# Performance work log

Measured on AMD Instinct MI355X. Metric: run time of the kernel, lower is better.

Reference implementation:

```python
import jax, jax.numpy as jnp
import numpy as np
from jax import lax

FEAT_STRIDE = 16
NMS_THRESH = 0.7
N_PRE = 6000   # test-mode n_test_pre_nms
N_POST = 300   # test-mode n_test_post_nms
MIN_SIZE = 16.0
SCALE = 1.0
RATIOS = (0.5, 1.0, 2.0)
ANCHOR_SCALES = (8, 16, 32)
BASE = 16
N_ANCHOR = len(RATIOS) * len(ANCHOR_SCALES)  # 9


def _anchor_base():
    py = px = BASE / 2.0
    ab = np.zeros((N_ANCHOR, 4), np.float32)
    for i, r in enumerate(RATIOS):
        for j, s in enumerate(ANCHOR_SCALES):
            h = BASE * s * np.sqrt(r)
            w = BASE * s * np.sqrt(1.0 / r)
            k = i * len(ANCHOR_SCALES) + j
            ab[k] = [py - h / 2.0, px - w / 2.0, py + h / 2.0, px + w / 2.0]
    return ab


def _anchors(hh, ww):
    # enumerate_shifted_anchor: (y1,x1,y2,x2) anchors for every feature cell
    ab = _anchor_base()
    sy = np.arange(0, hh * FEAT_STRIDE, FEAT_STRIDE)
    sx = np.arange(0, ww * FEAT_STRIDE, FEAT_STRIDE)
    SX, SY = np.meshgrid(sx, sy)
    shift = np.stack([SY.ravel(), SX.ravel(), SY.ravel(), SX.ravel()], 1)
    anc = (ab[None, :, :] + shift[:, None, :]).reshape(-1, 4).astype(np.float32)
    return jnp.asarray(anc)


def _iou(b):
    # b: [N,4] (y1,x1,y2,x2) -> [N,N] IoU
    y1, x1, y2, x2 = b[:, 0], b[:, 1], b[:, 2], b[:, 3]
    area = (y2 - y1) * (x2 - x1)
    ih = jnp.clip(jnp.minimum(y2[:, None], y2[None, :]) - jnp.maximum(y1[:, None], y1[None, :]), 0.0)
    iw = jnp.clip(jnp.minimum(x2[:, None], x2[None, :]) - jnp.maximum(x1[:, None], x1[None, :]), 0.0)
    inter = ih * iw
    return inter / (area[:, None] + area[None, :] - inter + 1e-9)


def _propose(loc, fg, anchor, img_h, img_w):
    # loc:[M,4] fg:[M] anchor:[M,4]  -> padded [N_POST,4] rois + valid mask
    ah = anchor[:, 2] - anchor[:, 0]
    aw = anchor[:, 3] - anchor[:, 1]
    acy = anchor[:, 0] + 0.5 * ah
    acx = anchor[:, 1] + 0.5 * aw
    cy = loc[:, 0] * ah + acy
    cx = loc[:, 1] * aw + acx
    h = jnp.exp(loc[:, 2]) * ah
    w = jnp.exp(loc[:, 3]) * aw
    roi = jnp.stack([
        jnp.clip(cy - 0.5 * h, 0.0, img_h),
        jnp.clip(cx - 0.5 * w, 0.0, img_w),
        jnp.clip(cy + 0.5 * h, 0.0, img_h),
        jnp.clip(cx + 0.5 * w, 0.0, img_w),
    ], axis=1)
    hs = roi[:, 2] - roi[:, 0]
    ws = roi[:, 3] - roi[:, 1]
    ms = MIN_SIZE * SCALE
    valid = (hs >= ms) & (ws >= ms)
    sc = jnp.where(valid, fg, -jnp.inf)  # drop too-small boxes from ranking
    top_sc, idx = lax.top_k(sc, N_PRE)   # score-sorted pre-NMS candidates
    boxes = roi[idx]
    ok = lax.stop_gradient(jnp.isfinite(top_sc))
    sup = lax.stop_gradient(_iou(boxes) > NMS_THRESH)  # [N_PRE,N_PRE]
    tri = jnp.arange(N_PRE)

    def body(i, keep):
        suppressed = jnp.any(keep & sup[:, i] & (tri < i))
        return keep.at[i].set(ok[i] & ~suppressed)

    keep = lax.fori_loop(0, N_PRE, body, jnp.zeros((N_PRE,), bool))
    rank = jnp.cumsum(keep.astype(jnp.int32)) - 1
    sel = keep & (rank < N_POST)
    tgt = jnp.where(sel, rank, N_POST)  # N_POST is out-of-bounds -> dropped
    out = jnp.zeros((N_POST, 4), boxes.dtype).at[tgt].set(boxes, mode='drop')
    vmask = jnp.zeros((N_POST,), bool).at[tgt].set(True, mode='drop')
    return out, vmask


def reference(x, conv1_w, conv1_b, score_w, score_b, loc_w, loc_b, img_h, img_w):
    n, _, hh, ww = x.shape
    anchor = _anchors(hh, ww)
    h = jax.nn.relu(
        lax.conv_general_dilated(x, conv1_w, (1, 1), 'SAME',
                                 dimension_numbers=('NCHW', 'OIHW', 'NCHW'))
        + conv1_b[None, :, None, None])
    locs = jnp.einsum('nchw,oc->nohw', h, loc_w[:, :, 0, 0]) + loc_b[None, :, None, None]
    scr = jnp.einsum('nchw,oc->nohw', h, score_w[:, :, 0, 0]) + score_b[None, :, None, None]
    rpn_locs = locs.transpose(0, 2, 3, 1).reshape(n, -1, 4)          # [n,M,4]
    scr_t = scr.transpose(0, 2, 3, 1)                                 # [n,hh,ww,2A]
    soft = jax.nn.softmax(scr_t.reshape(n, hh, ww, N_ANCHOR, 2), axis=-1)
    fg = soft[..., 1].reshape(n, -1)                                  # [n,M]
    rpn_scores = scr_t.reshape(n, -1, 2)
    rois, vmask = jax.vmap(lambda l, f: _propose(l, f, anchor, img_h, img_w))(rpn_locs, fg)
    roi_indices = jnp.broadcast_to(jnp.arange(n, dtype=jnp.int32)[:, None], (n, N_POST))
    return rpn_locs, rpn_scores, rois, roi_indices, anchor, vmask


def setup_inputs() -> dict:
    key = jax.random.key(0)
    ks = jax.random.split(key, 4)
    x = jax.random.normal(ks[0], (2, 512, 64, 64), jnp.float32)
    conv1_w = 0.01 * jax.random.normal(ks[1], (512, 512, 3, 3), jnp.float32)
    conv1_b = jnp.zeros((512,), jnp.float32)
    score_w = 0.01 * jax.random.normal(ks[2], (N_ANCHOR * 2, 512, 1, 1), jnp.float32)
    score_b = jnp.zeros((N_ANCHOR * 2,), jnp.float32)
    loc_w = 0.01 * jax.random.normal(ks[3], (N_ANCHOR * 4, 512, 1, 1), jnp.float32)
    loc_b = jnp.zeros((N_ANCHOR * 4,), jnp.float32)
    return {"x": x, "conv1_w": conv1_w, "conv1_b": conv1_b,
            "score_w": score_w, "score_b": score_b,
            "loc_w": loc_w, "loc_b": loc_b,
            "img_h": 1024, "img_w": 1024}
```

## Files before the change

kernel.cpp:

```cpp
#include <hip/hip_runtime.h>
#include <hip/hip_bf16.h>
#include <math.h>
#include <cstdint>

typedef unsigned long long u64;
typedef unsigned int u32;
typedef _Float16 half8 __attribute__((ext_vector_type(8)));
typedef float floatx4 __attribute__((ext_vector_type(4)));

#define NANCH 36864
#define SEG 65536
#define N_PRE 6000
#define N_POST 300
#define NW 96
#define NPADC 6144

#define O0 0
#define O1 294912
#define O2 442368
#define O3 444768
#define O4 445368
#define O5 592824

#define WS_XHI   0
#define WS_XLO   2097152
#define WS_WHI   4194304
#define WS_WLO   5373952
#define WS_WSLT  6553600
#define WS_WSLB  6586368
#define WS_H     6586432
#define WS_GUARD 10780736
#define WS_FG    0
#define WS_ROI   73728
#define WS_KEYS  368640
#define WS_SBOX  630784
#define WS_ALIVE 679936
#define WS_MASK  4194304

#define HSCALE 9.5367431640625e-07f

__device__ __forceinline__ void gl_lds16(const void* g, void* l) {
  __builtin_amdgcn_global_load_lds(
      (const __attribute__((address_space(1))) u32*)g,
      (__attribute__((address_space(3))) u32*)l, 16, 0, 0);
}

__device__ __forceinline__ u64 bcast64(u64 v, int src) {
  u32 lo = (u32)__shfl((int)(v & 0xFFFFFFFFull), src);
  u32 hi = (u32)__shfl((int)(v >> 32), src);
  return ((u64)hi << 32) | lo;
}

__global__ __launch_bounds__(256) void prep_all(
    const float* __restrict__ x, const float* __restrict__ w,
    const float* __restrict__ lw, const float* __restrict__ sw,
    const float* __restrict__ lb, const float* __restrict__ sb,
    float4* __restrict__ h, float4* __restrict__ guard,
    _Float16* __restrict__ xhi, _Float16* __restrict__ xlo,
    _Float16* __restrict__ whi, _Float16* __restrict__ wlo,
    float* __restrict__ wslt, float* __restrict__ wslb) {
  __shared__ float s[64 * 65];
  const int b = blockIdx.x, tid = threadIdx.x;
  if (b < 4097) {
    int idx = b * 256 + tid;
    if (idx < 1048576) h[idx] = make_float4(0.f, 0.f, 0.f, 0.f);
    else if (idx < 1048576 + 16) guard[idx - 1048576] = make_float4(0.f, 0.f, 0.f, 0.f);
    return;
  }
  if (b < 5121) {
    int l = b - 4097;
    int pt = l & 63, cg = (l >> 6) & 7, n = l >> 9;
    const int c0 = cg << 6, p0 = pt << 6;
#pragma unroll
    for (int kk = 0; kk < 16; ++kk) {
      int e = tid + (kk << 8);
      int ci = e >> 6, pi = e & 63;
      s[ci * 65 + pi] = x[(((size_t)(n * 512 + c0 + ci)) << 12) + p0 + pi];
    }
    __syncthreads();
#pragma unroll
    for (int kk = 0; kk < 16; ++kk) {
      int e = tid + (kk << 8);
      int ci = e & 63, pi = e >> 6;
      float sv = s[ci * 65 + pi] * 1024.f;
      _Float16 hi = (_Float16)sv;
      _Float16 lo = (_Float16)(sv - (float)hi);
      size_t off = (((size_t)(n << 12) + p0 + pi) << 9) + c0 + ci;
      xhi[off] = hi;
      xlo[off] = lo;
    }
    return;
  }
  if (b < 5697) {
    int l = b - 5121;
    int ct = l & 7, ot = (l >> 3) & 7, t = l >> 6;
    const int c0 = ct << 6, o0 = ot << 6;
#pragma unroll
    for (int kk = 0; kk < 16; ++kk) {
      int e = tid + (kk << 8);
      int ci = e & 63, oi = e >> 6;
      float sv = w[(size_t)(o0 + oi) * 4608 + (c0 + ci) * 9 + t] * 1024.f;
      _Float16 hi = (_Float16)sv;
      _Float16 lo = (_Float16)(sv - (float)hi);
      size_t off = ((size_t)((t << 9) + o0 + oi) << 9) + c0 + ci;
      whi[off] = hi;
      wlo[off] = lo;
    }
    return;
  }
  {
    int e = (b - 5697) * 256 + tid;
    if (e < 32768) {
      int c = e >> 6, o = e & 63;
      float v = 0.f;
      if (o < 36) v = lw[o * 512 + c];
      else if (o < 54) v = sw[(o - 36) * 512 + c];
      wslt[e] = v;
    } else if (e < 32832) {
      int o = e - 32768;
      float v = 0.f;
      if (o < 36) v = lb[o];
      else if (o < 54) v = sb[o - 36];
      wslb[o] = v;
    }
  }
}

__global__ __launch_bounds__(256) void conv_mfma(
    const _Float16* __restrict__ xhi, const _Float16* __restrict__ xlo,
    const _Float16* __restrict__ whi, const _Float16* __restrict__ wlo,
    const float* __restrict__ guard, float* __restrict__ hout) {
  __shared__ _Float16 aHi[4 * 68 * 32];
  __shared__ _Float16 aLo[4 * 68 * 32];
  __shared__ _Float16 bHi[128 * 32];
  __shared__ _Float16 bLo[128 * 32];
  const int tid = threadIdx.x;
  const int lane = tid & 63, w = tid >> 6;
  const int ptile = blockIdx.x;
  const int og = blockIdx.y;
  const int kq = blockIdx.z;
  const int n = ptile >> 5;
  const int y0 = (ptile & 31) << 1;
  const int o0 = og << 7;
  const int l15 = lane & 15, l16 = lane >> 4;
  const int ry = w >> 1;
  const int wo = (w & 1) << 6;

  floatx4 acc[4][4];
#pragma unroll
  for (int a = 0; a < 4; ++a)
#pragma unroll
    for (int b = 0; b < 4; ++b) acc[a][b] = (floatx4)0.f;

  for (int s = 0; s < 8; ++s) {
    const int c0 = (kq << 8) + (s << 5);
    __syncthreads();
    for (int i = w; i < 17; i += 4) {
      int chunk = (i << 6) + lane;
      int p = chunk >> 2, q = chunk & 3;
      int r = p / 68, xs = p - r * 68;
      int y = y0 - 1 + r, xg = xs - 1;
      bool ok = ((unsigned)y < 64u) && ((unsigned)xg < 64u);
      size_t off = (((size_t)(n << 12) + (y << 6) + xg) << 9) + c0 + (q << 3);
      const void* gh = ok ? (const void*)(xhi + off) : (const void*)guard;
      const void* gl = ok ? (const void*)(xlo + off) : (const void*)guard;
      gl_lds16(gh, (char*)aHi + (i << 10));
      gl_lds16(gl, (char*)aLo + (i << 10));
    }
    for (int tt = 0; tt < 9; ++tt) {
      if (tt > 0) __syncthreads();
      for (int i = w; i < 8; i += 4) {
        int chunk = (i << 6) + lane;
        int row = chunk >> 2, q = chunk & 3;
        size_t off = ((size_t)((tt << 9) + o0 + row) << 9) + c0 + (q << 3);
        gl_lds16((const void*)(whi + off), (char*)bHi + (i << 10));
        gl_lds16((const void*)(wlo + off), (char*)bLo + (i << 10));
      }
      __syncthreads();

      const int dy = tt / 3, dx = tt - 3 * dy;
      half8 ah[4], al[4], bh[4], bl[4];
#pragma unroll
      for (int im = 0; im < 4; ++im) {
        int xp = (im << 4) + l15;
        int p = (ry + dy) * 68 + xp + dx;
        ah[im] = *(const half8*)&aHi[(p << 5) + (l16 << 3)];
        al[im] = *(const half8*)&aLo[(p << 5) + (l16 << 3)];
      }
#pragma unroll
      for (int in = 0; in < 4; ++in) {
        int orow = wo + (in << 4) + l15;
        bh[in] = *(const half8*)&bHi[(orow << 5) + (l16 << 3)];
        bl[in] = *(const half8*)&bLo[(orow << 5) + (l16 << 3)];
      }
#pragma unroll
      for (int im = 0; im < 4; ++im)
#pragma unroll
        for (int in = 0; in < 4; ++in) {
          acc[im][in] = __builtin_amdgcn_mfma_f32_16x16x32_f16(
              ah[im], bh[in], acc[im][in], 0, 0, 0);
          acc[im][in] = __builtin_amdgcn_mfma_f32_16x16x32_f16(
              ah[im], bl[in], acc[im][in], 0, 0, 0);
          acc[im][in] = __builtin_amdgcn_mfma_f32_16x16x32_f16(
              al[im], bh[in], acc[im][in], 0, 0, 0);
        }
    }
  }

#pragma unroll
  for (int im = 0; im < 4; ++im)
#pragma unroll
    for (int in = 0; in < 4; ++in) {
      int o = o0 + wo + (in << 4) + l15;
#pragma unroll
      for (int reg = 0; reg < 4; ++reg) {
        int m_local = (ry << 6) + (im << 4) + (l16 << 2) + reg;
        size_t off = (((size_t)(n << 12) + (y0 << 6) + m_local) << 9) + o;
        atomicAdd(&hout[off], acc[im][in][reg]);
      }
    }
}

__global__ __launch_bounds__(256) void head_kernel(
    const float* __restrict__ hbuf, const float* __restrict__ cb,
    const float* __restrict__ wslt, const float* __restrict__ wslb,
    float* __restrict__ out, float* __restrict__ fgbuf) {
  const int y = blockIdx.x, n = blockIdx.y;
  __shared__ float sH[16 * 65];
  __shared__ float sWt[1024];
  __shared__ float sOut[64 * 65];
  const int tid = threadIdx.x;
  const int x = tid & 63, og = tid >> 6;

  float acc[16];
#pragma unroll
  for (int j = 0; j < 16; ++j) acc[j] = 0.f;

  const float* hb = hbuf + (((size_t)(n << 12) + (y << 6)) << 9);

  for (int c0 = 0; c0 < 512; c0 += 16) {
    __syncthreads();
#pragma unroll
    for (int p = 0; p < 4; ++p) {
      int e = tid + (p << 8);
      {
        int cc = e & 15, xx = e >> 4;
        float raw = hb[((size_t)xx << 9) + c0 + cc];
        sH[cc * 65 + xx] = fmaxf(raw * HSCALE + cb[c0 + cc], 0.f);
      }
      {
        int cc = e >> 6, xx = e & 63;
        sWt[e] = wslt[((c0 + cc) << 6) + xx];
      }
    }
    __syncthreads();
#pragma unroll
    for (int cc = 0; cc < 16; ++cc) {
      float hv = sH[cc * 65 + x];
      const float4* wp = (const float4*)&sWt[(cc << 6) + (og << 4)];
      float4 w0 = wp[0], w1 = wp[1], w2 = wp[2], w3 = wp[3];
      acc[0]  = fmaf(hv, w0.x, acc[0]);  acc[1]  = fmaf(hv, w0.y, acc[1]);
      acc[2]  = fmaf(hv, w0.z, acc[2]);  acc[3]  = fmaf(hv, w0.w, acc[3]);
      acc[4]  = fmaf(hv, w1.x, acc[4]);  acc[5]  = fmaf(hv, w1.y, acc[5]);
      acc[6]  = fmaf(hv, w1.z, acc[6]);  acc[7]  = fmaf(hv, w1.w, acc[7]);
      acc[8]  = fmaf(hv, w2.x, acc[8]);  acc[9]  = fmaf(hv, w2.y, acc[9]);
      acc[10] = fmaf(hv, w2.z, acc[10]); acc[11] = fmaf(hv, w2.w, acc[11]);
      acc[12] = fmaf(hv, w3.x, acc[12]); acc[13] = fmaf(hv, w3.y, acc[13]);
      acc[14] = fmaf(hv, w3.z, acc[14]); acc[15] = fmaf(hv, w3.w, acc[15]);
    }
  }
  __syncthreads();
#pragma unroll
  for (int j = 0; j < 16; ++j) {
    int o = (og << 4) + j;
    sOut[o * 65 + x] = acc[j] + wslb[o];
  }
  __syncthreads();

  const int p0 = (n << 12) + (y << 6);
  float* locs = out + O0 + (size_t)p0 * 36;
  for (int e = tid; e < 2304; e += 256) {
    int xx = e / 36, o = e - xx * 36;
    locs[e] = sOut[o * 65 + xx];
  }
  float* scrs = out + O1 + (size_t)p0 * 18;
  for (int e = tid; e < 1152; e += 256) {
    int xx = e / 18, ss = e - xx * 18;
    scrs[e] = sOut[(36 + ss) * 65 + xx];
  }
  float* fg = fgbuf + n * NANCH + (y << 6) * 9;
  for (int e = tid; e < 576; e += 256) {
    int xx = e / 9, a = e - xx * 9;
    float s0 = sOut[(36 + 2 * a) * 65 + xx];
    float s1 = sOut[(36 + 2 * a + 1) * 65 + xx];
    fg[e] = 1.0f / (1.0f + expf(s0 - s1));
  }
}

__global__ __launch_bounds__(256) void decode_kernel(
    const float* __restrict__ out0, const float* __restrict__ fgbuf,
    float4* __restrict__ roibuf, u64* __restrict__ keys,
    float* __restrict__ anchor_out, float* __restrict__ out,
    const int* __restrict__ imgh_p, const int* __restrict__ imgw_p) {
  int gid = blockIdx.x * 256 + threadIdx.x;
  if (gid < 3600) {
    if (gid < 2400) out[O2 + gid] = 0.f;
    else if (gid < 3000) out[O3 + (gid - 2400)] = (float)((gid - 2400) / 300);
    else out[O5 + (gid - 3000)] = 0.f;
  }
  int n = gid >> 16, k = gid & (SEG - 1);
  if (k >= NANCH) { keys[gid] = ~0ull; return; }
  int a = k % 9;
  int p = k / 9;
  int py = p >> 6, px = p & 63;

  const double R[3] = {0.5, 1.0, 2.0};
  const double S[3] = {8.0, 16.0, 32.0};
  double r = R[a / 3], s = S[a - (a / 3) * 3];
  double hd = 16.0 * s * sqrt(r);
  double wd = 16.0 * s * sqrt(1.0 / r);
  float ay1 = (float)(8.0 - hd / 2.0) + (float)(py * 16);
  float ax1 = (float)(8.0 - wd / 2.0) + (float)(px * 16);
  float ay2 = (float)(8.0 + hd / 2.0) + (float)(py * 16);
  float ax2 = (float)(8.0 + wd / 2.0) + (float)(px * 16);
  if (n == 0) {
    float* ao = anchor_out + (size_t)k * 4;
    ao[0] = ay1; ao[1] = ax1; ao[2] = ay2; ao[3] = ax2;
  }
  float ahk = ay2 - ay1, awk = ax2 - ax1;
  float acy = ay1 + 0.5f * ahk, acx = ax1 + 0.5f * awk;
  const float* lp = out0 + ((size_t)(n * NANCH + k) << 2);
  float dy = lp[0], dx = lp[1], dh = lp[2], dw = lp[3];
  float cy = dy * ahk + acy;
  float cx = dx * awk + acx;
  float bh = expf(dh) * ahk;
  float bw = expf(dw) * awk;
  float img_h = (float)imgh_p[0], img_w = (float)imgw_p[0];
  float y1 = fminf(fmaxf(cy - 0.5f * bh, 0.f), img_h);
  float x1 = fminf(fmaxf(cx - 0.5f * bw, 0.f), img_w);
  float y2 = fminf(fmaxf(cy + 0.5f * bh, 0.f), img_h);
  float x2 = fminf(fmaxf(cx + 0.5f * bw, 0.f), img_w);
  bool valid = ((y2 - y1) >= 16.f) && ((x2 - x1) >= 16.f);
  float sc = valid ? fgbuf[n * NANCH + k] : -INFINITY;
  roibuf[n * NANCH + k] = make_float4(y1, x1, y2, x2);
  unsigned int b = __float_as_uint(sc);
  unsigned int m = b ^ ((b & 0x80000000u) ? 0xFFFFFFFFu : 0x80000000u);
  keys[gid] = ((u64)(~m) << 32) | (unsigned int)k;
}

__global__ __launch_bounds__(256) void sort_local_a(u64* __restrict__ keys) {
  __shared__ u64 sk[4096];
  const int base = blockIdx.x << 12;
  for (int e = threadIdx.x; e < 4096; e += 256) sk[e] = keys[base + e];
  __syncthreads();
  for (int k = 2; k <= 4096; k <<= 1) {
    for (int j = k >> 1; j > 0; j >>= 1) {
      for (int t = threadIdx.x; t < 2048; t += 256) {
        int l = ((t & ~(j - 1)) << 1) | (t & (j - 1));
        int rr = l | j;
        bool asc = (((base + l) & k) == 0);
        u64 a = sk[l], b = sk[rr];
        if ((a > b) == asc) { sk[l] = b; sk[rr] = a; }
      }
      __syncthreads();
    }
  }
  for (int e = threadIdx.x; e < 4096; e += 256) keys[base + e] = sk[e];
}

__global__ __launch_bounds__(256) void sort_global_pass(u64* __restrict__ keys,
                                                        int k, int j) {
  int t = blockIdx.x * 256 + threadIdx.x;
  int l = ((t & ~(j - 1)) << 1) | (t & (j - 1));
  int rr = l | j;
  bool asc = (((l & (SEG - 1)) & k) == 0);
  u64 a = keys[l], b = keys[rr];
  if ((a > b) == asc) { keys[l] = b; keys[rr] = a; }
}

__global__ __launch_bounds__(256) void sort_global_pass2(u64* __restrict__ keys,
                                                         int k, int j1) {
  int t = blockIdx.x * 256 + threadIdx.x;
  int j2 = j1 >> 1;
  int l = ((t & ~(j2 - 1)) << 1) | (t & (j2 - 1));
  l = ((l & ~(j1 - 1)) << 1) | (l & (j1 - 1));
  u64 e0 = keys[l], e1 = keys[l | j2], e2 = keys[l | j1], e3 = keys[l | j1 | j2];
  bool asc = (((l & (SEG - 1)) & k) == 0);
  u64 tmp;
  if ((e0 > e2) == asc) { tmp = e0; e0 = e2; e2 = tmp; }
  if ((e1 > e3) == asc) { tmp = e1; e1 = e3; e3 = tmp; }
  if ((e0 > e1) == asc) { tmp = e0; e0 = e1; e1 = tmp; }
  if ((e2 > e3) == asc) { tmp = e2; e2 = e3; e3 = tmp; }
  keys[l] = e0; keys[l | j2] = e1; keys[l | j1] = e2; keys[l | j1 | j2] = e3;
}

__global__ __launch_bounds__(256) void sort_local_b(u64* __restrict__ keys, int k) {
  __shared__ u64 sk[4096];
  const int base = blockIdx.x << 12;
  for (int e = threadIdx.x; e < 4096; e += 256) sk[e] = keys[base + e];
  __syncthreads();
  for (int j = 2048; j > 0; j >>= 1) {
    for (int t = threadIdx.x; t < 2048; t += 256) {
      int l = ((t & ~(j - 1)) << 1) | (t & (j - 1));
      int rr = l | j;
      bool asc = ((((base + l) & (SEG - 1)) & k) == 0);
      u64 a = sk[l], b = sk[rr];
      if ((a > b) == asc) { sk[l] = b; sk[rr] = a; }
    }
    __syncthreads();
  }
  for (int e = threadIdx.x; e < 4096; e += 256) keys[base + e] = sk[e];
}

__global__ __launch_bounds__(256) void nms_gather(
    const u64* __restrict__ keys, const float4* __restrict__ roibuf,
    float4* __restrict__ sbox, u64* __restrict__ alive) {
  const int n = blockIdx.y;
  int i = blockIdx.x * 256 + threadIdx.x;
  u64 kk = (i < N_PRE) ? keys[(n << 16) + i] : ~0ull;
  bool valid = ((unsigned)(kk >> 32)) < 0xFF800000u;
  float4 b = make_float4(0.f, 0.f, 0.f, 0.f);
  if (valid) b = roibuf[(size_t)n * NANCH + (unsigned)(kk & 0xFFFFFFFFull)];
  sbox[n * NPADC + i] = b;
  u64 bal = __ballot(valid);
  if ((threadIdx.x & 63) == 0) alive[n * NW + (i >> 6)] = bal;
}

__global__ __launch_bounds__(256) void build_mask(
    const float4* __restrict__ sbox, u64* __restrict__ M) {
  __shared__ float4 jb[4][64];
  __shared__ float ja[4][64];
  const int tid = threadIdx.x, lane = tid & 63, wv = tid >> 6;
  const int g = blockIdx.x, q = blockIdx.y, n = blockIdx.z;
  const float4* sb = sbox + n * NPADC;
  float4 bi = sb[(g << 6) + lane];
  float ai = (bi.z - bi.x) * (bi.w - bi.y);
  u64* Mrow = M + ((size_t)(n * NPADC + (g << 6) + lane)) * NW;
#pragma unroll
  for (int it = 0; it < 6; ++it) {
    int w = q * 24 + (it << 2) + wv;
    float4 bjl = sb[(w << 6) + lane];
    jb[wv][lane] = bjl;
    ja[wv][lane] = (bjl.z - bjl.x) * (bjl.w - bjl.y);
    u64 bits = 0;
#pragma unroll 8
    for (int j = 0; j < 64; ++j) {
      float4 bj = jb[wv][j];
      float aj = ja[wv][j];
      float ih = fmaxf(fminf(bi.z, bj.z) - fmaxf(bi.x, bj.x), 0.f);
      float iw = fmaxf(fminf(bi.w, bj.w) - fmaxf(bi.y, bj.y), 0.f);
      float inter = ih * iw;
      bool bit = inter / (ai + aj - inter + 1e-9f) > 0.7f;
      bits |= ((u64)bit) << j;
    }
    Mrow[w] = bits;
  }
}

__global__ __launch_bounds__(64) void nms_reduce(
    const u64* __restrict__ M, const u64* __restrict__ alive,
    const float4* __restrict__ sbox, float* __restrict__ out) {
  const int n = blockIdx.x, lane = threadIdx.x;
  float* rois = out + O2 + n * (N_POST * 4);
  float* vmask = out + O5 + n * N_POST;
  const u64* A = alive + n * NW;
  const u64* Mb = M + (size_t)n * NPADC * NW;
  const float4* sb = sbox + n * NPADC;
  u64 aw0 = A[lane];
  u64 aw1 = (lane < 32) ? A[64 + lane] : 0ull;
  u64 accA = 0, accB = 0;
  int nk = 0;
  u64 dnext = Mb[(size_t)lane * NW + 0];
  float4 bnext = sb[lane];
  const u64 below = lane ? (~0ull >> (64 - lane)) : 0ull;

  for (int c = 0; c < 94; ++c) {
    u64 dcur = dnext;
    float4 bcur = bnext;
    if (c + 1 < 94) {
      dnext = Mb[(size_t)(((c + 1) << 6) + lane) * NW + (c + 1)];
      bnext = sb[((c + 1) << 6) + lane];
    }
    u64 wacc = (c < 64) ? bcast64(accA, c) : bcast64(accB, c - 64);
    u64 aw = (c < 64) ? bcast64(aw0, c) : bcast64(aw1, c - 64);
    u64 alive_u = aw & ~wacc;
    if (alive_u == 0ull) continue;

    u64 dmask = dcur & below;
    u64 rem = alive_u, kept = 0;
    while (rem) {
      int j = __builtin_ctzll(rem);
      kept |= 1ull << j;
      u64 col = __ballot((dmask >> j) & 1);
      rem &= ~(col | (1ull << j));
    }

    int npop = __popcll(kept);
    if ((kept >> lane) & 1ull) {
      int slot = nk + __popcll(kept & below);
      if (slot < N_POST) {
        rois[slot * 4 + 0] = bcur.x; rois[slot * 4 + 1] = bcur.y;
        rois[slot * 4 + 2] = bcur.z; rois[slot * 4 + 3] = bcur.w;
        vmask[slot] = 1.0f;
      }
    }
    if (nk + npop >= N_POST) break;
    nk += npop;

    u64 kk = kept;
    while (kk) {
      int j0 = __builtin_ctzll(kk); kk &= kk - 1;
      int j1 = kk ? __builtin_ctzll(kk) : j0; kk &= kk - 1;
      int j2 = kk ? __builtin_ctzll(kk) : j0; kk &= kk - 1;
      int j3 = kk ? __builtin_ctzll(kk) : j0; kk &= kk - 1;
      int j4 = kk ? __builtin_ctzll(kk) : j0; kk &= kk - 1;
      int j5 = kk ? __builtin_ctzll(kk) : j0; kk &= kk - 1;
      int j6 = kk ? __builtin_ctzll(kk) : j0; kk &= kk - 1;
      int j7 = kk ? __builtin_ctzll(kk) : j0; kk &= kk - 1;
      const u64* r0 = Mb + (size_t)((c << 6) + j0) * NW;
      const u64* r1 = Mb + (size_t)((c << 6) + j1) * NW;
      const u64* r2 = Mb + (size_t)((c << 6) + j2) * NW;
      const u64* r3 = Mb + (size_t)((c << 6) + j3) * NW;
      const u64* r4 = Mb + (size_t)((c << 6) + j4) * NW;
      const u64* r5 = Mb + (size_t)((c << 6) + j5) * NW;
      const u64* r6 = Mb + (size_t)((c << 6) + j6) * NW;
      const u64* r7 = Mb + (size_t)((c << 6) + j7) * NW;
      u64 oA = r0[lane] | r1[lane] | r2[lane] | r3[lane]
             | r4[lane] | r5[lane] | r6[lane] | r7[lane];
      u64 oB = 0;
      if (lane < 32)
        oB = r0[64 + lane] | r1[64 + lane] | r2[64 + lane] | r3[64 + lane]
           | r4[64 + lane] | r5[64 + lane] | r6[64 + lane] | r7[64 + lane];
      accA |= oA;
      accB |= oB;
    }
  }
}

extern "C" void kernel_launch(void* const* d_in, const int* in_sizes, int n_in,
                              void* d_out, int out_size, void* d_ws, size_t ws_size,
                              hipStream_t stream) {
  const float* x        = (const float*)d_in[0];
  const float* conv1_w  = (const float*)d_in[1];
  const float* conv1_b  = (const float*)d_in[2];
  const float* score_w  = (const float*)d_in[3];
  const float* score_b  = (const float*)d_in[4];
  const float* loc_w    = (const float*)d_in[5];
  const float* loc_b    = (const float*)d_in[6];
  const int*   imgh_p   = (const int*)d_in[7];
  const int*   imgw_p   = (const int*)d_in[8];

  float* out = (float*)d_out;
  float* ws  = (float*)d_ws;

  _Float16* xhi = (_Float16*)(ws + WS_XHI);
  _Float16* xlo = (_Float16*)(ws + WS_XLO);
  _Float16* whi = (_Float16*)(ws + WS_WHI);
  _Float16* wlo = (_Float16*)(ws + WS_WLO);
  float* wslt   = ws + WS_WSLT;
  float* wslb   = ws + WS_WSLB;
  float* hbuf   = ws + WS_H;
  float* guard  = ws + WS_GUARD;
  float* fgbuf   = ws + WS_FG;
  float4* roibuf = (float4*)(ws + WS_ROI);
  u64* keys      = (u64*)(ws + WS_KEYS);
  float4* sbox   = (float4*)(ws + WS_SBOX);
  u64* alive     = (u64*)(ws + WS_ALIVE);
  u64* maskbuf   = (u64*)(ws + WS_MASK);

  prep_all<<<5826, 256, 0, stream>>>(x, conv1_w, loc_w, score_w, loc_b, score_b,
                                     (float4*)hbuf, (float4*)guard,
                                     xhi, xlo, whi, wlo, wslt, wslb);

  conv_mfma<<<dim3(64, 4, 2), 256, 0, stream>>>(xhi, xlo, whi, wlo, guard, hbuf);

  head_kernel<<<dim3(64, 2), 256, 0, stream>>>(hbuf, conv1_b, wslt, wslb, out, fgbuf);
  decode_kernel<<<512, 256, 0, stream>>>(out, fgbuf, roibuf, keys,
                                         out + O4, out, imgh_p, imgw_p);

  sort_local_a<<<32, 256, 0, stream>>>(keys);
  for (int k = 8192; k <= SEG; k <<= 1) {
    int j = k >> 1;
    while (j >= 4096) {
      if (j >= 8192) {
        sort_global_pass2<<<128, 256, 0, stream>>>(keys, k, j);
        j >>= 2;
      } else {
        sort_global_pass<<<256, 256, 0, stream>>>(keys, k, j);
        j >>= 1;
      }
    }
    sort_local_b<<<32, 256, 0, stream>>>(keys, k);
  }

  nms_gather<<<dim3(24, 2), 256, 0, stream>>>(keys, roibuf, sbox, alive);
  build_mask<<<dim3(96, 4, 2), 256, 0, stream>>>(sbox, maskbuf);
  nms_reduce<<<2, 64, 0, stream>>>(maskbuf, alive, sbox, out);
}
```

Measured before the change: 499.2 us.

## Replace full bitonic sort with histogram top-k select; swizzle conv LDS, split-K 4

Swaps the multi-launch 65536-element global bitonic sort for a pass that builds a radix histogram of score keys, scans it to find the cutoff bin for the top 6000, compacts the survivors and sorts 8192 keys in one LDS block per image, gathering boxes in the same kernel. Separately, the conv kernel splits the reduction over 4 K-chunks instead of 2 and XOR-style swizzles the LDS layout to cut bank conflicts. The head kernel now uses float4 loads and zeroes the histogram and key buffers. This removes many kernel launches and a lot of global-memory sort traffic. In exchange it adds more atomics on the conv output and relies on at most 8192 candidates falling at or below the cutoff bin, so ties could be truncated.

```diff
diff --git a/kernel.cpp b/kernel.cpp
--- a/kernel.cpp
+++ b/kernel.cpp
@@ -35,6 +35,10 @@
 #define WS_KEYS  368640
 #define WS_SBOX  630784
 #define WS_ALIVE 679936
+#define WS_CKEYS 680320
+#define WS_CNT   717184
+#define WS_CUT   717248
+#define WS_HIST2 2097152
 #define WS_MASK  4194304
 
 #define HSCALE 9.5367431640625e-07f
@@ -139,8 +143,8 @@
   const int ptile = blockIdx.x;
   const int og = blockIdx.y;
   const int kq = blockIdx.z;
-  const int n = ptile >> 5;
   const int y0 = (ptile & 31) << 1;
+  const int nimg = ptile >> 5;
   const int o0 = og << 7;
   const int l15 = lane & 15, l16 = lane >> 4;
   const int ry = w >> 1;
@@ -152,16 +156,17 @@
 #pragma unroll
     for (int b = 0; b < 4; ++b) acc[a][b] = (floatx4)0.f;
 
-  for (int s = 0; s < 8; ++s) {
-    const int c0 = (kq << 8) + (s << 5);
+  for (int s = 0; s < 4; ++s) {
+    const int c0 = (kq << 7) + (s << 5);
     __syncthreads();
     for (int i = w; i < 17; i += 4) {
       int chunk = (i << 6) + lane;
-      int p = chunk >> 2, q = chunk & 3;
+      int p = chunk >> 2;
+      int q = ((chunk & 3) - ((chunk >> 3) & 3)) & 3;
       int r = p / 68, xs = p - r * 68;
       int y = y0 - 1 + r, xg = xs - 1;
       bool ok = ((unsigned)y < 64u) && ((unsigned)xg < 64u);
-      size_t off = (((size_t)(n << 12) + (y << 6) + xg) << 9) + c0 + (q << 3);
+      size_t off = (((size_t)(nimg << 12) + (y << 6) + xg) << 9) + c0 + (q << 3);
       const void* gh = ok ? (const void*)(xhi + off) : (const void*)guard;
       const void* gl = ok ? (const void*)(xlo + off) : (const void*)guard;
       gl_lds16(gh, (char*)aHi + (i << 10));
@@ -171,7 +176,8 @@
       if (tt > 0) __syncthreads();
       for (int i = w; i < 8; i += 4) {
         int chunk = (i << 6) + lane;
-        int row = chunk >> 2, q = chunk & 3;
+        int row = chunk >> 2;
+        int q = ((chunk & 3) - ((chunk >> 3) & 3)) & 3;
         size_t off = ((size_t)((tt << 9) + o0 + row) << 9) + c0 + (q << 3);
         gl_lds16((const void*)(whi + off), (char*)bHi + (i << 10));
         gl_lds16((const void*)(wlo + off), (char*)bLo + (i << 10));
@@ -183,15 +189,17 @@
 #pragma unroll
       for (int im = 0; im < 4; ++im) {
         int xp = (im << 4) + l15;
-        int p = (ry + dy) * 68 + xp + dx;
-        ah[im] = *(const half8*)&aHi[(p << 5) + (l16 << 3)];
-        al[im] = *(const half8*)&aLo[(p << 5) + (l16 << 3)];
+        int P = (ry + dy) * 68 + xp + dx;
+        int sw = ((l16 + (P >> 1)) & 3) << 3;
+        ah[im] = *(const half8*)&aHi[(P << 5) + sw];
+        al[im] = *(const half8*)&aLo[(P << 5) + sw];
       }
 #pragma unroll
       for (int in = 0; in < 4; ++in) {
         int orow = wo + (in << 4) + l15;
-        bh[in] = *(const half8*)&bHi[(orow << 5) + (l16 << 3)];
-        bl[in] = *(const half8*)&bLo[(orow << 5) + (l16 << 3)];
+        int swb = ((l16 + (orow >> 1)) & 3) << 3;
+        bh[in] = *(const half8*)&bHi[(orow << 5) + swb];
+        bl[in] = *(const half8*)&bLo[(orow << 5) + swb];
       }
 #pragma unroll
       for (int im = 0; im < 4; ++im)
@@ -215,7 +223,7 @@
 #pragma unroll
       for (int reg = 0; reg < 4; ++reg) {
         int m_local = (ry << 6) + (im << 4) + (l16 << 2) + reg;
-        size_t off = (((size_t)(n << 12) + (y0 << 6) + m_local) << 9) + o;
+        size_t off = (((size_t)(nimg << 12) + (y0 << 6) + m_local) << 9) + o;
         atomicAdd(&hout[off], acc[im][in][reg]);
       }
     }
@@ -224,13 +232,25 @@
 __global__ __launch_bounds__(256) void head_kernel(
     const float* __restrict__ hbuf, const float* __restrict__ cb,
     const float* __restrict__ wslt, const float* __restrict__ wslb,
-    float* __restrict__ out, float* __restrict__ fgbuf) {
+    float* __restrict__ out, float* __restrict__ fgbuf,
+    float4* __restrict__ zkeys, float4* __restrict__ zhist,
+    float4* __restrict__ zcnt) {
   const int y = blockIdx.x, n = blockIdx.y;
   __shared__ float sH[16 * 65];
   __shared__ float sWt[1024];
   __shared__ float sOut[64 * 65];
   const int tid = threadIdx.x;
   const int x = tid & 63, og = tid >> 6;
+  const int bb = (n << 6) + y;
+
+  {
+    float f = __uint_as_float(0xFFFFFFFFu);
+    if (tid < 64) zkeys[(bb << 6) + tid] = make_float4(f, f, f, f);
+#pragma unroll
+    for (int i = 0; i < 4; ++i)
+      zhist[(bb << 10) + (i << 8) + tid] = make_float4(0.f, 0.f, 0.f, 0.f);
+    if (bb == 0 && tid < 16) zcnt[tid] = make_float4(0.f, 0.f, 0.f, 0.f);
+  }
 
   float acc[16];
 #pragma unroll
@@ -238,20 +258,17 @@
 
   const float* hb = hbuf + (((size_t)(n << 12) + (y << 6)) << 9);
 
+  const int cc4 = (tid & 3) << 2, xx = tid >> 2;
   for (int c0 = 0; c0 < 512; c0 += 16) {
     __syncthreads();
-#pragma unroll
-    for (int p = 0; p < 4; ++p) {
-      int e = tid + (p << 8);
-      {
-        int cc = e & 15, xx = e >> 4;
-        float raw = hb[((size_t)xx << 9) + c0 + cc];
-        sH[cc * 65 + xx] = fmaxf(raw * HSCALE + cb[c0 + cc], 0.f);
-      }
-      {
-        int cc = e >> 6, xx = e & 63;
-        sWt[e] = wslt[((c0 + cc) << 6) + xx];
-      }
+    {
+      float4 v = *(const float4*)&hb[((size_t)xx << 9) + c0 + cc4];
+      float4 bbv = *(const float4*)&cb[c0 + cc4];
+      sH[(cc4 + 0) * 65 + xx] = fmaxf(v.x * HSCALE + bbv.x, 0.f);
+      sH[(cc4 + 1) * 65 + xx] = fmaxf(v.y * HSCALE + bbv.y, 0.f);
+      sH[(cc4 + 2) * 65 + xx] = fmaxf(v.z * HSCALE + bbv.z, 0.f);
+      sH[(cc4 + 3) * 65 + xx] = fmaxf(v.w * HSCALE + bbv.w, 0.f);
+      *(float4*)&sWt[tid << 2] = *(const float4*)&wslt[(c0 << 6) + (tid << 2)];
     }
     __syncthreads();
 #pragma unroll
@@ -280,19 +297,19 @@
   const int p0 = (n << 12) + (y << 6);
   float* locs = out + O0 + (size_t)p0 * 36;
   for (int e = tid; e < 2304; e += 256) {
-    int xx = e / 36, o = e - xx * 36;
-    locs[e] = sOut[o * 65 + xx];
+    int xp = e / 36, o = e - xp * 36;
+    locs[e] = sOut[o * 65 + xp];
   }
   float* scrs = out + O1 + (size_t)p0 * 18;
   for (int e = tid; e < 1152; e += 256) {
-    int xx = e / 18, ss = e - xx * 18;
-    scrs[e] = sOut[(36 + ss) * 65 + xx];
+    int xp = e / 18, ss = e - xp * 18;
+    scrs[e] = sOut[(36 + ss) * 65 + xp];
   }
   float* fg = fgbuf + n * NANCH + (y << 6) * 9;
   for (int e = tid; e < 576; e += 256) {
-    int xx = e / 9, a = e - xx * 9;
-    float s0 = sOut[(36 + 2 * a) * 65 + xx];
-    float s1 = sOut[(36 + 2 * a + 1) * 65 + xx];
+    int xp = e / 9, a = e - xp * 9;
+    float s0 = sOut[(36 + 2 * a) * 65 + xp];
+    float s1 = sOut[(36 + 2 * a + 1) * 65 + xp];
     fg[e] = 1.0f / (1.0f + expf(s0 - s1));
   }
 }
@@ -301,15 +318,18 @@
     const float* __restrict__ out0, const float* __restrict__ fgbuf,
     float4* __restrict__ roibuf, u64* __restrict__ keys,
     float* __restrict__ anchor_out, float* __restrict__ out,
+    u32* __restrict__ ghist,
     const int* __restrict__ imgh_p, const int* __restrict__ imgw_p) {
-  int gid = blockIdx.x * 256 + threadIdx.x;
+  const int tid = threadIdx.x, bb = blockIdx.x;
+  const int n = bb / 144;
+  const int k = (bb - n * 144) * 256 + tid;
+  int gid = bb * 256 + tid;
   if (gid < 3600) {
     if (gid < 2400) out[O2 + gid] = 0.f;
     else if (gid < 3000) out[O3 + (gid - 2400)] = (float)((gid - 2400) / 300);
     else out[O5 + (gid - 3000)] = 0.f;
   }
-  int n = gid >> 16, k = gid & (SEG - 1);
-  if (k >= NANCH) { keys[gid] = ~0ull; return; }
+
   int a = k % 9;
   int p = k / 9;
   int py = p >> 6, px = p & 63;
@@ -345,85 +365,83 @@
   roibuf[n * NANCH + k] = make_float4(y1, x1, y2, x2);
   unsigned int b = __float_as_uint(sc);
   unsigned int m = b ^ ((b & 0x80000000u) ? 0xFFFFFFFFu : 0x80000000u);
-  keys[gid] = ((u64)(~m) << 32) | (unsigned int)k;
-}
-
-__global__ __launch_bounds__(256) void sort_local_a(u64* __restrict__ keys) {
-  __shared__ u64 sk[4096];
-  const int base = blockIdx.x << 12;
-  for (int e = threadIdx.x; e < 4096; e += 256) sk[e] = keys[base + e];
+  u32 hi = ~m;
+  keys[(n << 16) + k] = ((u64)hi << 32) | (unsigned int)k;
+  atomicAdd(&ghist[(n << 18) + (hi >> 14)], 1u);
+}
+
+__global__ __launch_bounds__(1024) void scan_cut(const u32* __restrict__ ghist,
+                                                 u32* __restrict__ cut) {
+  __shared__ u32 ps[1024];
+  const int n = blockIdx.x, tid = threadIdx.x;
+  const u32* h = ghist + (n << 18);
+  u32 s = 0;
+  const uint4* h4 = (const uint4*)(h + (tid << 8));
+#pragma unroll
+  for (int i = 0; i < 64; ++i) {
+    uint4 v = h4[i];
+    s += v.x + v.y + v.z + v.w;
+  }
+  ps[tid] = s;
   __syncthreads();
-  for (int k = 2; k <= 4096; k <<= 1) {
+  for (int off = 1; off < 1024; off <<= 1) {
+    u32 v = (tid >= off) ? ps[tid - off] : 0;
+    __syncthreads();
+    ps[tid] += v;
+    __syncthreads();
+  }
+  u32 cumEnd = ps[tid], cumStart = cumEnd - s;
+  if (cumStart < N_PRE && cumEnd >= N_PRE) {
+    u32 c = cumStart;
+    for (int i = 0; i < 256; ++i) {
+      c += h[(tid << 8) + i];
+      if (c >= N_PRE) { cut[n] = (tid << 8) + i; break; }
+    }
+  }
+}
+
+__global__ __launch_bounds__(256) void compact(
+    const u64* __restrict__ keys, const u32* __restrict__ cut,
+    u32* __restrict__ cnt, u64* __restrict__ ckeys) {
+  const int b = blockIdx.x;
+  const int n = b / 144;
+  const int k = (b - n * 144) * 256 + threadIdx.x;
+  u64 key = keys[(n << 16) + k];
+  u32 bin = (u32)(key >> 46);
+  if (bin <= cut[n]) {
+    u32 pos = atomicAdd(&cnt[n], 1u);
+    if (pos < 8192) ckeys[(n << 13) + pos] = key;
+  }
+}
+
+__global__ __launch_bounds__(1024) void sort8k(
+    const u64* __restrict__ ckeys, const float4* __restrict__ roibuf,
+    float4* __restrict__ sbox, u64* __restrict__ alive) {
+  __shared__ u64 sk[8192];
+  const int n = blockIdx.x, tid = threadIdx.x;
+  for (int i = tid; i < 8192; i += 1024) sk[i] = ckeys[(n << 13) + i];
+  __syncthreads();
+  for (int k = 2; k <= 8192; k <<= 1) {
     for (int j = k >> 1; j > 0; j >>= 1) {
-      for (int t = threadIdx.x; t < 2048; t += 256) {
+      for (int t = tid; t < 4096; t += 1024) {
         int l = ((t & ~(j - 1)) << 1) | (t & (j - 1));
         int rr = l | j;
-        bool asc = (((base + l) & k) == 0);
+        bool asc = ((l & k) == 0);
         u64 a = sk[l], b = sk[rr];
         if ((a > b) == asc) { sk[l] = b; sk[rr] = a; }
       }
       __syncthreads();
     }
   }
-  for (int e = threadIdx.x; e < 4096; e += 256) keys[base + e] = sk[e];
-}
-
-__global__ __launch_bounds__(256) void sort_global_pass(u64* __restrict__ keys,
-                                                        int k, int j) {
-  int t = blockIdx.x * 256 + threadIdx.x;
-  int l = ((t & ~(j - 1)) << 1) | (t & (j - 1));
-  int rr = l | j;
-  bool asc = (((l & (SEG - 1)) & k) == 0);
-  u64 a = keys[l], b = keys[rr];
-  if ((a > b) == asc) { keys[l] = b; keys[rr] = a; }
-}
-
-__global__ __launch_bounds__(256) void sort_global_pass2(u64* __restrict__ keys,
-                                                         int k, int j1) {
-  int t = blockIdx.x * 256 + threadIdx.x;
-  int j2 = j1 >> 1;
-  int l = ((t & ~(j2 - 1)) << 1) | (t & (j2 - 1));
-  l = ((l & ~(j1 - 1)) << 1) | (l & (j1 - 1));
-  u64 e0 = keys[l], e1 = keys[l | j2], e2 = keys[l | j1], e3 = keys[l | j1 | j2];
-  bool asc = (((l & (SEG - 1)) & k) == 0);
-  u64 tmp;
-  if ((e0 > e2) == asc) { tmp = e0; e0 = e2; e2 = tmp; }
-  if ((e1 > e3) == asc) { tmp = e1; e1 = e3; e3 = tmp; }
-  if ((e0 > e1) == asc) { tmp = e0; e0 = e1; e1 = tmp; }
-  if ((e2 > e3) == asc) { tmp = e2; e2 = e3; e3 = tmp; }
-  keys[l] = e0; keys[l | j2] = e1; keys[l | j1] = e2; keys[l | j1 | j2] = e3;
-}
-
-__global__ __launch_bounds__(256) void sort_local_b(u64* __restrict__ keys, int k) {
-  __shared__ u64 sk[4096];
-  const int base = blockIdx.x << 12;
-  for (int e = threadIdx.x; e < 4096; e += 256) sk[e] = keys[base + e];
-  __syncthreads();
-  for (int j = 2048; j > 0; j >>= 1) {
-    for (int t = threadIdx.x; t < 2048; t += 256) {
-      int l = ((t & ~(j - 1)) << 1) | (t & (j - 1));
-      int rr = l | j;
-      bool asc = ((((base + l) & (SEG - 1)) & k) == 0);
-      u64 a = sk[l], b = sk[rr];
-      if ((a > b) == asc) { sk[l] = b; sk[rr] = a; }
-    }
-    __syncthreads();
-  }
-  for (int e = threadIdx.x; e < 4096; e += 256) keys[base + e] = sk[e];
-}
-
-__global__ __launch_bounds__(256) void nms_gather(
-    const u64* __restrict__ keys, const float4* __restrict__ roibuf,
-    float4* __restrict__ sbox, u64* __restrict__ alive) {
-  const int n = blockIdx.y;
-  int i = blockIdx.x * 256 + threadIdx.x;
-  u64 kk = (i < N_PRE) ? keys[(n << 16) + i] : ~0ull;
-  bool valid = ((unsigned)(kk >> 32)) < 0xFF800000u;
-  float4 b = make_float4(0.f, 0.f, 0.f, 0.f);
-  if (valid) b = roibuf[(size_t)n * NANCH + (unsigned)(kk & 0xFFFFFFFFull)];
-  sbox[n * NPADC + i] = b;
-  u64 bal = __ballot(valid);
-  if ((threadIdx.x & 63) == 0) alive[n * NW + (i >> 6)] = bal;
+  for (int i = tid; i < NPADC; i += 1024) {
+    u64 kk = sk[i];
+    bool valid = (i < N_PRE) && (((u32)(kk >> 32)) < 0xFF800000u);
+    float4 b = make_float4(0.f, 0.f, 0.f, 0.f);
+    if (valid) b = roibuf[(size_t)n * NANCH + (u32)(kk & 0xFFFFFFFFull)];
+    sbox[n * NPADC + i] = b;
+    u64 bal = __ballot(valid);
+    if ((tid & 63) == 0) alive[n * NW + (i >> 6)] = bal;
+  }
 }
 
 __global__ __launch_bounds__(256) void build_mask(
@@ -566,34 +584,27 @@
   u64* keys      = (u64*)(ws + WS_KEYS);
   float4* sbox   = (float4*)(ws + WS_SBOX);
   u64* alive     = (u64*)(ws + WS_ALIVE);
+  u64* ckeys     = (u64*)(ws + WS_CKEYS);
+  u32* cnt       = (u32*)(ws + WS_CNT);
+  u32* cut       = (u32*)(ws + WS_CUT);
+  u32* ghist     = (u32*)(ws + WS_HIST2);
   u64* maskbuf   = (u64*)(ws + WS_MASK);
 
   prep_all<<<5826, 256, 0, stream>>>(x, conv1_w, loc_w, score_w, loc_b, score_b,
                                      (float4*)hbuf, (float4*)guard,
                                      xhi, xlo, whi, wlo, wslt, wslb);
 
-  conv_mfma<<<dim3(64, 4, 2), 256, 0, stream>>>(xhi, xlo, whi, wlo, guard, hbuf);
-
-  head_kernel<<<dim3(64, 2), 256, 0, stream>>>(hbuf, conv1_b, wslt, wslb, out, fgbuf);
-  decode_kernel<<<512, 256, 0, stream>>>(out, fgbuf, roibuf, keys,
-                                         out + O4, out, imgh_p, imgw_p);
-
-  sort_local_a<<<32, 256, 0, stream>>>(keys);
-  for (int k = 8192; k <= SEG; k <<= 1) {
-    int j = k >> 1;
-    while (j >= 4096) {
-      if (j >= 8192) {
-        sort_global_pass2<<<128, 256, 0, stream>>>(keys, k, j);
-        j >>= 2;
-      } else {
-        sort_global_pass<<<256, 256, 0, stream>>>(keys, k, j);
-        j >>= 1;
-      }
-    }
-    sort_local_b<<<32, 256, 0, stream>>>(keys, k);
-  }
-
-  nms_gather<<<dim3(24, 2), 256, 0, stream>>>(keys, roibuf, sbox, alive);
+  conv_mfma<<<dim3(64, 4, 4), 256, 0, stream>>>(xhi, xlo, whi, wlo, guard, hbuf);
+
+  head_kernel<<<dim3(64, 2), 256, 0, stream>>>(hbuf, conv1_b, wslt, wslb, out,
+                                               fgbuf, (float4*)ckeys,
+                                               (float4*)ghist, (float4*)cnt);
+  decode_kernel<<<288, 256, 0, stream>>>(out, fgbuf, roibuf, keys,
+                                         out + O4, out, ghist, imgh_p, imgw_p);
+  scan_cut<<<2, 1024, 0, stream>>>(ghist, cut);
+  compact<<<288, 256, 0, stream>>>(keys, cut, cnt, ckeys);
+  sort8k<<<2, 1024, 0, stream>>>(ckeys, roibuf, sbox, alive);
+
   build_mask<<<dim3(96, 4, 2), 256, 0, stream>>>(sbox, maskbuf);
   nms_reduce<<<2, 64, 0, stream>>>(maskbuf, alive, sbox, out);
 }
```

Result: slower. 531.3 us (+6.4%).
